# Kernel tuning notes

Measured on AMD Instinct MI355X. Metric: run time of the kernel, lower is better.

The kernel has to match this reference:

```python
import jax, jax.numpy as jnp
import numpy as np

L, S, N, E, H = 1024, 1024, 8, 1024, 16

def setup_inputs() -> dict:
    key = jax.random.key(0)
    k0, k1, k2, k3 = jax.random.split(key, 4)
    query = jax.random.normal(k0, (L, N, E), jnp.float32)
    key_t = jax.random.normal(k1, (S, N, E), jnp.float32)
    in_proj_weight = jax.random.normal(k2, (3 * E, E), jnp.float32) * (1.0 / np.sqrt(E))
    in_proj_bias = jnp.zeros((3 * E,), jnp.float32)
    attn_bias = jax.random.normal(k3, (N * H, L, S), jnp.float32) * 0.02
    return {"query": query, "key": key_t, "in_proj_weight": in_proj_weight,
            "in_proj_bias": in_proj_bias, "attn_bias": attn_bias}

def reference(query, key, in_proj_weight, in_proj_bias, attn_bias):
    tgt_len, bsz, embed_dim = query.shape
    head_dim = embed_dim // H
    scaling = float(head_dim) ** -0.5  # scale_factor = 1
    # q/k projections: first two embed_dim-row slices of in_proj_weight
    q = query @ in_proj_weight[:embed_dim].T + in_proj_bias[:embed_dim]
    k = key @ in_proj_weight[embed_dim:2 * embed_dim].T + in_proj_bias[embed_dim:2 * embed_dim]
    q = q * scaling
    # (L, N, E) -> (N*H, L, hd)
    q = q.reshape(tgt_len, bsz * H, head_dim).transpose(1, 0, 2)
    k = k.reshape(-1, bsz * H, head_dim).transpose(1, 0, 2)
    # scores: (N*H, L, S), additive bias, then stable softmax
    scores = jnp.einsum('bld,bsd->bls', q, k) + attn_bias
    attn_output_weights = jax.nn.softmax(scores, axis=-1)
    return attn_output_weights
```

## Files before the change

kernel.cpp:

```cpp
#include <hip/hip_runtime.h>
#include <hip/hip_bf16.h>
#include <stdint.h>

#define L_DIM 1024
#define S_DIM 1024
#define N_DIM 8
#define E_DIM 1024
#define H_DIM 16
#define HD    64
#define BH    (N_DIM*H_DIM)
#define M_ROWS (L_DIM*N_DIM)

#define AS1 __attribute__((address_space(1)))
#define AS3 __attribute__((address_space(3)))

typedef __bf16 bf16x8 __attribute__((ext_vector_type(8)));
typedef float  f32x4  __attribute__((ext_vector_type(4)));
typedef _Float16 f16;
typedef _Float16 f16x8 __attribute__((ext_vector_type(8)));
typedef unsigned short u16;
typedef unsigned short u16x8 __attribute__((ext_vector_type(8)));

__device__ inline u16 f2bf(float x){
  unsigned int u = __float_as_uint(x);
  u = (u + 0x7FFFu + ((u >> 16) & 1u)) >> 16;
  return (u16)u;
}

__global__ __launch_bounds__(256) void convert_kernel(
    const float* __restrict__ query, const float* __restrict__ key,
    const float* __restrict__ w,
    u16* __restrict__ qbf, u16* __restrict__ kbf,
    u16* __restrict__ wq, u16* __restrict__ wk)
{
  const int QN = M_ROWS*E_DIM;
  const int WN = E_DIM*E_DIM;
  const int total8 = (2*QN + 2*WN)/8;
  int stride = gridDim.x*blockDim.x;
  for (int g = blockIdx.x*blockDim.x + threadIdx.x; g < total8; g += stride) {
    int base = g*8;
    const float* src; u16* dst; float scale = 1.0f;
    if (base < QN)           { src = query + base;      dst = qbf + base; }
    else if (base < 2*QN)    { src = key + (base-QN);   dst = kbf + (base-QN); }
    else if (base < 2*QN+WN) { src = w + (base-2*QN);   dst = wq + (base-2*QN); scale = 0.125f; }
    else                     { src = w + (base-2*QN);   dst = wk + (base-2*QN-WN); }
    float4 v0 = *(const float4*)(src);
    float4 v1 = *(const float4*)(src+4);
    u16x8 o;
    o[0]=f2bf(v0.x*scale); o[1]=f2bf(v0.y*scale); o[2]=f2bf(v0.z*scale); o[3]=f2bf(v0.w*scale);
    o[4]=f2bf(v1.x*scale); o[5]=f2bf(v1.y*scale); o[6]=f2bf(v1.z*scale); o[7]=f2bf(v1.w*scale);
    *(u16x8*)dst = o;
  }
}

__global__ __launch_bounds__(256) void proj_gemm(
    const u16* __restrict__ A, const u16* __restrict__ W,
    const float* __restrict__ bias, float bscale,
    u16* __restrict__ C)
{
  __shared__ __align__(16) u16 As[128*32];
  __shared__ __align__(16) u16 Bs[128*32];
  const int t = threadIdx.x;
  const int lane = t & 63;
  const int w = t >> 6;
  const int wr = w >> 1, wc = w & 1;
  const int rowTile = blockIdx.x * 128;
  const int colTile = blockIdx.y * 128;

  f32x4 acc[4][4];
  #pragma unroll
  for (int m=0;m<4;m++)
    #pragma unroll
    for (int n=0;n<4;n++) acc[m][n] = (f32x4){0.f,0.f,0.f,0.f};

  uint32_t asBase = (uint32_t)(uintptr_t)&As[0];
  uint32_t bsBase = (uint32_t)(uintptr_t)&Bs[0];
  const char* Ab = (const char*)A;
  const char* Wb = (const char*)W;

  for (int kt = 0; kt < 32; ++kt) {
    __syncthreads();
    #pragma unroll
    for (int issue = 0; issue < 2; ++issue) {
      int o = issue*4096 + t*16;
      int row  = o >> 6;
      int colb = o & 63;
      const char* ga = Ab + (size_t)(rowTile + row)*2048 + kt*64 + colb;
      const char* gb = Wb + (size_t)(colTile + row)*2048 + kt*64 + colb;
      uint32_t la = asBase + issue*4096 + (w<<10);
      uint32_t lb = bsBase + issue*4096 + (w<<10);
      __builtin_amdgcn_global_load_lds(
          (const AS1 void*)(uintptr_t)ga, (AS3 void*)(uintptr_t)la, 16, 0, 0);
      __builtin_amdgcn_global_load_lds(
          (const AS1 void*)(uintptr_t)gb, (AS3 void*)(uintptr_t)lb, 16, 0, 0);
    }
    __syncthreads();

    bf16x8 af[4], bfr[4];
    int krow = (lane >> 4) * 16;
    #pragma unroll
    for (int m=0;m<4;m++) {
      int r = wr*64 + m*16 + (lane&15);
      af[m] = *(const bf16x8*)((const char*)As + r*64 + krow);
    }
    #pragma unroll
    for (int n=0;n<4;n++) {
      int r = wc*64 + n*16 + (lane&15);
      bfr[n] = *(const bf16x8*)((const char*)Bs + r*64 + krow);
    }
    #pragma unroll
    for (int m=0;m<4;m++)
      #pragma unroll
      for (int n=0;n<4;n++)
        acc[m][n] = __builtin_amdgcn_mfma_f32_16x16x32_bf16(af[m], bfr[n], acc[m][n], 0,0,0);
  }

  #pragma unroll
  for (int n2=0;n2<4;n2++) {
    int gcol = colTile + wc*64 + n2*16 + (lane&15);
    int h = gcol >> 6, d = gcol & 63;
    float bv = bias[gcol]*bscale;
    #pragma unroll
    for (int m=0;m<4;m++) {
      int grow0 = rowTile + wr*64 + m*16 + ((lane>>4)<<2);
      #pragma unroll
      for (int r=0;r<4;r++) {
        int grow = grow0 + r;
        int l = grow >> 3, nn = grow & 7;
        C[((size_t)(nn*16 + h)*1024 + l)*64 + d] = f2bf(acc[m][n2][r] + bv);
      }
    }
  }
}

__global__ __launch_bounds__(256) void attn_softmax(
    const u16* __restrict__ Qh, const u16* __restrict__ Kh,
    const float* __restrict__ bias, float* __restrict__ out)
{
  __shared__ __align__(16) char scb[16*2048];
  __shared__ __align__(16) char kbuf[8192];
  const int t = threadIdx.x;
  const int lane = t & 63;
  const int w = t >> 6;
  const int ltile = blockIdx.x;
  const int b = blockIdx.y;

  const char* Kb = (const char*)(Kh + (size_t)b*1024*64);
  const u16*  Qb = Qh + (size_t)b*1024*64 + (size_t)ltile*16*64;

  int qoff = (lane&15)*64 + (lane>>4)*8;
  bf16x8 a0 = *(const bf16x8*)(Qb + qoff);
  bf16x8 a1 = *(const bf16x8*)(Qb + qoff + 32);

  const int rowBase = (lane>>4)*4;
  uint32_t kbase = (uint32_t)(uintptr_t)&kbuf[0];

  for (int g = 0; g < 16; ++g) {
    __syncthreads();
    #pragma unroll
    for (int rd = 0; rd < 2; ++rd) {
      int o = rd*4096 + t*16;
      int src = o ^ (((o>>7)&7)<<4);
      __builtin_amdgcn_global_load_lds(
          (const AS1 void*)(uintptr_t)(Kb + (size_t)g*8192 + src),
          (AS3 void*)(uintptr_t)(kbase + rd*4096 + (w<<10)), 16, 0, 0);
    }
    __syncthreads();

    int r = w*16 + (lane&15);
    int byte0 = r*128 + ((lane>>4)*16);
    int swzk = (r&7)<<4;
    bf16x8 b0 = *(const bf16x8*)(kbuf + ((byte0      ) ^ swzk));
    bf16x8 b1 = *(const bf16x8*)(kbuf + ((byte0 + 64 ) ^ swzk));
    f32x4 acc = {0.f,0.f,0.f,0.f};
    acc = __builtin_amdgcn_mfma_f32_16x16x32_bf16(a0, b0, acc, 0,0,0);
    acc = __builtin_amdgcn_mfma_f32_16x16x32_bf16(a1, b1, acc, 0,0,0);

    int scol = g*64 + w*16 + (lane & 15);
    #pragma unroll
    for (int rr=0;rr<4;rr++) {
      int row = rowBase + rr;
      int byte = (row*2048 + scol*2) ^ ((row&7)<<4);
      *(f16*)(scb + byte) = (f16)acc[rr];
    }
  }
  __syncthreads();

  #pragma unroll
  for (int rr=0;rr<4;rr++) {
    int row = rr*4 + w;
    int l_glob = ltile*16 + row;
    const float* brow = bias + ((size_t)b*1024 + l_glob)*1024;
    float*       orow = out  + ((size_t)b*1024 + l_glob)*1024;
    const int swz = (row&7)<<4;
    float v[16];
    float mx = -1e30f;
    #pragma unroll
    for (int it=0; it<2; ++it) {
      int cb = it*1024 + lane*16;
      f16x8 s8 = *(const f16x8*)(scb + ((row*2048 + cb) ^ swz));
      int col = it*512 + lane*8;
      f32x4 b4a = *(const f32x4*)(brow + col);
      f32x4 b4b = *(const f32x4*)(brow + col + 4);
      #pragma unroll
      for (int j=0;j<4;j++) v[it*8+j]   = (float)s8[j]   + b4a[j];
      #pragma unroll
      for (int j=0;j<4;j++) v[it*8+4+j] = (float)s8[4+j] + b4b[j];
    }
    #pragma unroll
    for (int j=0;j<16;j++) mx = fmaxf(mx, v[j]);
    #pragma unroll
    for (int off=32; off>0; off>>=1) mx = fmaxf(mx, __shfl_xor(mx, off, 64));
    float sum = 0.f;
    #pragma unroll
    for (int j=0;j<16;j++) { v[j] = __expf(v[j]-mx); sum += v[j]; }
    #pragma unroll
    for (int off=32; off>0; off>>=1) sum += __shfl_xor(sum, off, 64);
    float inv = 1.0f / sum;
    #pragma unroll
    for (int it=0; it<2; ++it) {
      int col = it*512 + lane*8;
      f32x4 o4a = { v[it*8+0]*inv, v[it*8+1]*inv, v[it*8+2]*inv, v[it*8+3]*inv };
      f32x4 o4b = { v[it*8+4]*inv, v[it*8+5]*inv, v[it*8+6]*inv, v[it*8+7]*inv };
      *(f32x4*)(orow + col)     = o4a;
      *(f32x4*)(orow + col + 4) = o4b;
    }
  }
}

extern "C" void kernel_launch(void* const* d_in, const int* in_sizes, int n_in,
                              void* d_out, int out_size, void* d_ws, size_t ws_size,
                              hipStream_t stream) {
  const float* query = (const float*)d_in[0];
  const float* key   = (const float*)d_in[1];
  const float* w     = (const float*)d_in[2];
  const float* bias  = (const float*)d_in[3];
  const float* abias = (const float*)d_in[4];
  float* out = (float*)d_out;

  char* ws = (char*)d_ws;
  const size_t QKB = (size_t)M_ROWS*E_DIM*2;
  const size_t WB  = (size_t)E_DIM*E_DIM*2;
  u16* qbf = (u16*)ws;  ws += QKB;
  u16* kbf = (u16*)ws;  ws += QKB;
  u16* wq  = (u16*)ws;  ws += WB;
  u16* wk  = (u16*)ws;  ws += WB;
  u16* Qh  = (u16*)ws;  ws += QKB;
  u16* Kh  = (u16*)ws;  ws += QKB;

  hipLaunchKernelGGL(convert_kernel, dim3(2048), dim3(256), 0, stream,
                     query, key, w, qbf, kbf, wq, wk);
  hipLaunchKernelGGL(proj_gemm, dim3(64, 8), dim3(256), 0, stream,
                     qbf, wq, bias, 0.125f, Qh);
  hipLaunchKernelGGL(proj_gemm, dim3(64, 8), dim3(256), 0, stream,
                     kbf, wk, bias + 1024, 1.0f, Kh);
  hipLaunchKernelGGL(attn_softmax, dim3(64, 128), dim3(256), 0, stream,
                     Qh, Kh, abias, out);
}
```

Before: 322.3 us.

## Merge Q/K projections into one launch and load K directly in attention

The two projection GEMMs become a single launch that uses blockIdx.z to pick Q or K, cutting one kernel launch and letting both GEMMs share the GPU. The attention kernel drops the LDS staging of K and its per-step barriers: each wave reads its K rows straight from global memory and swaps the MFMA operands so that four scores are written as one packed f16x4 store. The grid is flattened and remapped so that consecutive workgroups go to different XCDs while workgroups sharing a head land on the same one, which is meant to improve L2 reuse of K. The bias is read with nontemporal loads so that it does not evict reused data from cache.

```diff
diff --git a/kernel.cpp b/kernel.cpp
--- a/kernel.cpp
+++ b/kernel.cpp
@@ -17,6 +17,7 @@
 typedef __bf16 bf16x8 __attribute__((ext_vector_type(8)));
 typedef float  f32x4  __attribute__((ext_vector_type(4)));
 typedef _Float16 f16;
+typedef _Float16 f16x4 __attribute__((ext_vector_type(4)));
 typedef _Float16 f16x8 __attribute__((ext_vector_type(8)));
 typedef unsigned short u16;
 typedef unsigned short u16x8 __attribute__((ext_vector_type(8)));
@@ -54,10 +55,18 @@
 }
 
 __global__ __launch_bounds__(256) void proj_gemm(
-    const u16* __restrict__ A, const u16* __restrict__ W,
-    const float* __restrict__ bias, float bscale,
-    u16* __restrict__ C)
+    const u16* __restrict__ Aq, const u16* __restrict__ Wq_,
+    const u16* __restrict__ Ak, const u16* __restrict__ Wk_,
+    const float* __restrict__ bias_all,
+    u16* __restrict__ Cq, u16* __restrict__ Ck)
 {
+  const int z = blockIdx.z;
+  const u16* A = z ? Ak : Aq;
+  const u16* W = z ? Wk_ : Wq_;
+  const float* bias = bias_all + z*1024;
+  const float bscale = z ? 1.0f : 0.125f;
+  u16* C = z ? Ck : Cq;
+
   __shared__ __align__(16) u16 As[128*32];
   __shared__ __align__(16) u16 Bs[128*32];
   const int t = threadIdx.x;
@@ -138,51 +147,36 @@
     const float* __restrict__ bias, float* __restrict__ out)
 {
   __shared__ __align__(16) char scb[16*2048];
-  __shared__ __align__(16) char kbuf[8192];
   const int t = threadIdx.x;
   const int lane = t & 63;
   const int w = t >> 6;
-  const int ltile = blockIdx.x;
-  const int b = blockIdx.y;
-
-  const char* Kb = (const char*)(Kh + (size_t)b*1024*64);
-  const u16*  Qb = Qh + (size_t)b*1024*64 + (size_t)ltile*16*64;
+  int wg = blockIdx.x;
+  int swz = (wg & 7) * 1024 + (wg >> 3);
+  const int b = swz >> 6;
+  const int ltile = swz & 63;
+
+  const u16* Kb = Kh + (size_t)b*1024*64;
+  const u16* Qb = Qh + (size_t)b*1024*64 + (size_t)ltile*16*64;
 
   int qoff = (lane&15)*64 + (lane>>4)*8;
   bf16x8 a0 = *(const bf16x8*)(Qb + qoff);
   bf16x8 a1 = *(const bf16x8*)(Qb + qoff + 32);
 
-  const int rowBase = (lane>>4)*4;
-  uint32_t kbase = (uint32_t)(uintptr_t)&kbuf[0];
-
-  for (int g = 0; g < 16; ++g) {
-    __syncthreads();
-    #pragma unroll
-    for (int rd = 0; rd < 2; ++rd) {
-      int o = rd*4096 + t*16;
-      int src = o ^ (((o>>7)&7)<<4);
-      __builtin_amdgcn_global_load_lds(
-          (const AS1 void*)(uintptr_t)(Kb + (size_t)g*8192 + src),
-          (AS3 void*)(uintptr_t)(kbase + rd*4096 + (w<<10)), 16, 0, 0);
-    }
-    __syncthreads();
-
-    int r = w*16 + (lane&15);
-    int byte0 = r*128 + ((lane>>4)*16);
-    int swzk = (r&7)<<4;
-    bf16x8 b0 = *(const bf16x8*)(kbuf + ((byte0      ) ^ swzk));
-    bf16x8 b1 = *(const bf16x8*)(kbuf + ((byte0 + 64 ) ^ swzk));
+  const u16* Kw = Kb + (size_t)w*16*1024;
+  const int kfo = (lane&15)*64 + (lane>>4)*8;
+  const int q = lane & 15;
+  const int qswz = (q & 7) << 4;
+  #pragma unroll 4
+  for (int st = 0; st < 16; ++st) {
+    const u16* kp = Kw + st*1024 + kfo;
+    bf16x8 b0 = *(const bf16x8*)kp;
+    bf16x8 b1 = *(const bf16x8*)(kp + 32);
     f32x4 acc = {0.f,0.f,0.f,0.f};
-    acc = __builtin_amdgcn_mfma_f32_16x16x32_bf16(a0, b0, acc, 0,0,0);
-    acc = __builtin_amdgcn_mfma_f32_16x16x32_bf16(a1, b1, acc, 0,0,0);
-
-    int scol = g*64 + w*16 + (lane & 15);
-    #pragma unroll
-    for (int rr=0;rr<4;rr++) {
-      int row = rowBase + rr;
-      int byte = (row*2048 + scol*2) ^ ((row&7)<<4);
-      *(f16*)(scb + byte) = (f16)acc[rr];
-    }
+    acc = __builtin_amdgcn_mfma_f32_16x16x32_bf16(b0, a0, acc, 0,0,0);
+    acc = __builtin_amdgcn_mfma_f32_16x16x32_bf16(b1, a1, acc, 0,0,0);
+    int sbase = (w*16 + st)*16 + ((lane>>4)<<2);
+    f16x4 sv = { (f16)acc[0], (f16)acc[1], (f16)acc[2], (f16)acc[3] };
+    *(f16x4*)(scb + ((q*2048 + sbase*2) ^ qswz)) = sv;
   }
   __syncthreads();
 
@@ -192,16 +186,16 @@
     int l_glob = ltile*16 + row;
     const float* brow = bias + ((size_t)b*1024 + l_glob)*1024;
     float*       orow = out  + ((size_t)b*1024 + l_glob)*1024;
-    const int swz = (row&7)<<4;
+    const int rswz = (row&7)<<4;
     float v[16];
     float mx = -1e30f;
     #pragma unroll
     for (int it=0; it<2; ++it) {
       int cb = it*1024 + lane*16;
-      f16x8 s8 = *(const f16x8*)(scb + ((row*2048 + cb) ^ swz));
+      f16x8 s8 = *(const f16x8*)(scb + ((row*2048 + cb) ^ rswz));
       int col = it*512 + lane*8;
-      f32x4 b4a = *(const f32x4*)(brow + col);
-      f32x4 b4b = *(const f32x4*)(brow + col + 4);
+      f32x4 b4a = __builtin_nontemporal_load((const f32x4*)(brow + col));
+      f32x4 b4b = __builtin_nontemporal_load((const f32x4*)(brow + col + 4));
       #pragma unroll
       for (int j=0;j<4;j++) v[it*8+j]   = (float)s8[j]   + b4a[j];
       #pragma unroll
@@ -250,10 +244,8 @@
 
   hipLaunchKernelGGL(convert_kernel, dim3(2048), dim3(256), 0, stream,
                      query, key, w, qbf, kbf, wq, wk);
-  hipLaunchKernelGGL(proj_gemm, dim3(64, 8), dim3(256), 0, stream,
-                     qbf, wq, bias, 0.125f, Qh);
-  hipLaunchKernelGGL(proj_gemm, dim3(64, 8), dim3(256), 0, stream,
-                     kbf, wk, bias + 1024, 1.0f, Kh);
-  hipLaunchKernelGGL(attn_softmax, dim3(64, 128), dim3(256), 0, stream,
+  hipLaunchKernelGGL(proj_gemm, dim3(64, 8, 2), dim3(256), 0, stream,
+                     qbf, wq, kbf, wk, bias, Qh, Kh);
+  hipLaunchKernelGGL(attn_softmax, dim3(8192), dim3(256), 0, stream,
                      Qh, Kh, abias, out);
 }
```

Result: slower. 379.5 us (+17.7%).
